# Optimization experiments

Hardware: AMD Instinct MI355X
Metric: run time of the kernel (lower is better)

Reference implementation:

```python
import jax, jax.numpy as jnp
import numpy as np

C = 256
CQK = C // 8  # query/key channels from Conv2d(in_dim, in_dim//8, 1)


def _cross_attn(x, y, qw, qb, kw, kb, vw, vb, gamma):
    # x, y: [B, C, H, W]; 1x1 convs are channel matmuls
    B, Cc, H, W = x.shape
    N = H * W
    xf = x.reshape(B, Cc, N)
    yf = y.reshape(B, Cc, N)
    q = jnp.einsum('oc,bcn->bno', qw, xf) + qb  # [B, N, CQK]
    k = jnp.einsum('oc,bcn->bon', kw, yf) + kb[:, None]  # [B, CQK, N]
    energy = jnp.einsum('bnc,bcm->bnm', q, k)  # [B, N, N]
    attn = jax.nn.softmax(energy, axis=2)
    v = jnp.einsum('oc,bcn->bon', vw, yf) + vb[:, None]  # [B, C, N]
    out = jnp.einsum('bcm,bnm->bcn', v, attn)  # value @ attention^T
    out = out.reshape(B, Cc, H, W)
    return gamma * out + x


def setup_inputs() -> dict:
    key = jax.random.key(0)
    ks = jax.random.split(key, 16)
    B, H, W = 4, 64, 64
    s = 1.0 / np.sqrt(C)
    d = {
        'x': jax.random.normal(ks[0], (B, C, H, W), jnp.float32),
        'y': jax.random.normal(ks[1], (B, C, H, W), jnp.float32),
        'z': jax.random.normal(ks[2], (B, C, H, W), jnp.float32),
        'q1_w': jax.random.normal(ks[3], (CQK, C), jnp.float32) * s,
        'q1_b': jax.random.normal(ks[4], (CQK,), jnp.float32) * s,
        'k1_w': jax.random.normal(ks[5], (CQK, C), jnp.float32) * s,
        'k1_b': jax.random.normal(ks[6], (CQK,), jnp.float32) * s,
        'v1_w': jax.random.normal(ks[7], (C, C), jnp.float32) * s,
        'v1_b': jax.random.normal(ks[8], (C,), jnp.float32) * s,
        'gamma1': jax.random.normal(ks[9], (1,), jnp.float32) * 0.1,
        'q2_w': jax.random.normal(ks[10], (CQK, C), jnp.float32) * s,
        'q2_b': jax.random.normal(ks[11], (CQK,), jnp.float32) * s,
        'k2_w': jax.random.normal(ks[12], (CQK, C), jnp.float32) * s,
        'k2_b': jax.random.normal(ks[13], (CQK,), jnp.float32) * s,
        'v2_w': jax.random.normal(ks[14], (C, C), jnp.float32) * s,
        'v2_b': jax.random.normal(ks[15], (C,), jnp.float32) * s,
        'gamma2': jax.random.normal(jax.random.fold_in(key, 99), (1,), jnp.float32) * 0.1,
    }
    return d


def reference(x, y, z, q1_w, q1_b, k1_w, k1_b, v1_w, v1_b, gamma1,
              q2_w, q2_b, k2_w, k2_b, v2_w, v2_b, gamma2):
    out1 = _cross_attn(x, y, q1_w, q1_b, k1_w, k1_b, v1_w, v1_b, gamma1)
    out2 = _cross_attn(out1, z, q2_w, q2_b, k2_w, k2_b, v2_w, v2_b, gamma2)
    return out2
```

## Files before the change

### kernel.cpp

```cpp
#include <hip/hip_runtime.h>
#include <hip/hip_bf16.h>

#define NSEQ 4096
#define CDIM 256
#define CQKD 32
#define LOG2E 1.4426950408889634f

typedef float v4f __attribute__((ext_vector_type(4)));
typedef float v16f __attribute__((ext_vector_type(16)));
typedef short v8s __attribute__((ext_vector_type(8)));
typedef unsigned long long u64;

__device__ __forceinline__ float exp2_(float x) {
#if __has_builtin(__builtin_amdgcn_exp2f)
  return __builtin_amdgcn_exp2f(x);
#else
  float r;
  __asm__("v_exp_f32 %0, %1" : "=v"(r) : "v"(x));
  return r;
#endif
}

__device__ __forceinline__ unsigned short f2bf(float x) {
  unsigned u = __builtin_bit_cast(unsigned, x);
  unsigned r = (u + 0x7FFFu + ((u >> 16) & 1u)) >> 16;
  return (unsigned short)r;
}
__device__ __forceinline__ float bf2f(unsigned short s) {
  unsigned u = ((unsigned)s) << 16;
  return __builtin_bit_cast(float, u);
}
__device__ __forceinline__ unsigned int pack_bf16(float a, float b) {
#if __has_builtin(__builtin_amdgcn_cvt_pk_bf16_f32)
  typedef __bf16 v2bf __attribute__((ext_vector_type(2)));
  v2bf r = __builtin_amdgcn_cvt_pk_bf16_f32(a, b);
  return __builtin_bit_cast(unsigned int, r);
#else
  return ((unsigned)f2bf(b) << 16) | (unsigned)f2bf(a);
#endif
}

__device__ __forceinline__ unsigned char f2e4m3(float x) {
  unsigned u = __builtin_bit_cast(unsigned, x);
  unsigned s = (u >> 24) & 0x80u;
  unsigned au = u & 0x7fffffffu;
  if (au > 0x43e00000u) return (unsigned char)(s | 0x7eu);
  if (au < 0x3c800000u) {
    float ax = __builtin_bit_cast(float, au);
    int q = (int)(ax * 512.0f + 0.5f);
    if (q > 7) q = 7;
    return (unsigned char)(s | (unsigned)q);
  }
  int e = (int)((au >> 23) & 0xffu) - 127 + 7;
  unsigned m = au & 0x7fffffu;
  unsigned mr = m + 0x7ffffu + ((m >> 20) & 1u);
  if (mr >= 0x800000u) { mr -= 0x800000u; e += 1; if (e >= 16) return (unsigned char)(s | 0x7e); }
  return (unsigned char)(s | ((unsigned)e << 3) | (mr >> 20));
}
__device__ __forceinline__ unsigned int pack4_fp8(float a, float b, float c, float d) {
#if __has_builtin(__builtin_amdgcn_cvt_pk_fp8_f32)
  int v = 0;
  v = __builtin_amdgcn_cvt_pk_fp8_f32(a, b, v, false);
  v = __builtin_amdgcn_cvt_pk_fp8_f32(c, d, v, true);
  return (unsigned int)v;
#else
  return (unsigned)f2e4m3(a) | ((unsigned)f2e4m3(b) << 8) |
         ((unsigned)f2e4m3(c) << 16) | ((unsigned)f2e4m3(d) << 24);
#endif
}

__device__ __forceinline__ void barrier_lds() {
  __asm__ __volatile__("s_waitcnt lgkmcnt(0)\n\ts_barrier" ::: "memory");
}

__global__ __launch_bounds__(256) void convw_kernel(
    const float* __restrict__ q1w, const float* __restrict__ k1w,
    const float* __restrict__ k2w, const float* __restrict__ q2w,
    const float* __restrict__ v1w, const float* __restrict__ v2w,
    unsigned short* __restrict__ W) {
  const int s = blockIdx.x * 256 + threadIdx.x;
  const float* src;
  int o, ch0;
  size_t obase;
  float scale = 1.0f;
  if (s < 3072) {
    const int wsel = s >> 10, r = s & 1023;
    src = wsel == 0 ? q1w : (wsel == 1 ? k1w : k2w);
    const int ot = r >> 9, cb = (r >> 6) & 7, lane = r & 63;
    o = ot * 16 + (lane & 15);
    ch0 = cb * 32 + ((lane >> 4) & 3) * 8;
    obase = (size_t)wsel * 8192 + (size_t)r * 8;
  } else if (s < 19456) {
    const int s2 = s - 3072, which = s2 >> 13, r = s2 & 8191;
    src = which == 0 ? v1w : v2w;
    const int ot = r >> 9, cb = (r >> 6) & 7, lane = r & 63;
    o = ot * 16 + (lane & 15);
    ch0 = cb * 32 + ((lane >> 4) & 3) * 8;
    obase = 32768 + (size_t)which * 65536 + (size_t)r * 8;
  } else {
    const int r = s - 19456;
    src = q2w;
    const int lane = r & 63;
    o = lane & 31;
    ch0 = (r >> 6) * 16 + (lane >> 5) * 8;
    obase = 24576 + (size_t)r * 8;
    scale = LOG2E;
  }
#pragma unroll
  for (int j = 0; j < 8; ++j)
    W[obase + j] = f2bf(src[o * CDIM + ch0 + j] * scale);
}

__global__ __launch_bounds__(256) void prep_kernel(
    const float* __restrict__ x, const float* __restrict__ y,
    const float* __restrict__ z, const unsigned short* __restrict__ Wbf,
    const float* __restrict__ q1b, const float* __restrict__ k1b,
    const float* __restrict__ k2b, const float* __restrict__ v1b,
    const float* __restrict__ v2b, unsigned short* __restrict__ Q1,
    unsigned short* __restrict__ K1, unsigned short* __restrict__ K2,
    unsigned char* __restrict__ V1, unsigned char* __restrict__ V2) {
  __shared__ unsigned short t[256][72];
  __shared__ unsigned short Kt[64][40];
  const int src = blockIdx.z;
  const float* in = src == 0 ? x : (src == 1 ? y : z);
  const int b = blockIdx.y;
  const int n0 = blockIdx.x * 64;
  const int tid = threadIdx.x, lane = tid & 63, w = tid >> 6;
  const int quad = lane >> 4, r15 = lane & 15, l31 = lane & 31, lh = lane >> 5;
  const float* ip = in + (size_t)(b * CDIM) * NSEQ + n0;
  {
    const int chb = tid >> 4, c4 = (tid & 15) * 4;
#pragma unroll
    for (int p = 0; p < 16; ++p) {
      const int ch = p * 16 + chb;
      float4 v = *(const float4*)(ip + (size_t)ch * NSEQ + c4);
      uint2 pk;
      pk.x = pack_bf16(v.x, v.y);
      pk.y = pack_bf16(v.z, v.w);
      *(uint2*)&t[ch][c4] = pk;
    }
  }
  __syncthreads();
  v8s af[8];
#pragma unroll
  for (int cb = 0; cb < 8; ++cb) {
    union { unsigned short e[8]; v8s v; } u;
#pragma unroll
    for (int j = 0; j < 8; ++j) u.e[j] = t[cb * 32 + quad * 8 + j][w * 16 + r15];
    af[cb] = u.v;
  }
  const int nt = blockIdx.x * 4 + w;
  const unsigned short* Wqk = Wbf + src * 8192;
  v4f a0 = {0.f, 0.f, 0.f, 0.f}, a1 = a0;
#pragma unroll
  for (int cb = 0; cb < 8; ++cb) {
    v8s b0 = *(const v8s*)(Wqk + (size_t)cb * 512 + lane * 8);
    v8s b1 = *(const v8s*)(Wqk + (size_t)(8 + cb) * 512 + lane * 8);
    a0 = __builtin_amdgcn_mfma_f32_16x16x32_bf16(af[cb], b0, a0, 0, 0, 0);
    a1 = __builtin_amdgcn_mfma_f32_16x16x32_bf16(af[cb], b1, a1, 0, 0, 0);
  }
  if (src == 0) {
#pragma unroll
    for (int r = 0; r < 4; ++r) {
      Q1[((size_t)b * NSEQ + nt * 16 + quad * 4 + r) * CQKD + r15] =
          f2bf((a0[r] + q1b[r15]) * LOG2E);
      Q1[((size_t)b * NSEQ + nt * 16 + quad * 4 + r) * CQKD + 16 + r15] =
          f2bf((a1[r] + q1b[16 + r15]) * LOG2E);
    }
    return;
  }
  const float* kbias = src == 1 ? k1b : k2b;
#pragma unroll
  for (int r = 0; r < 4; ++r) {
    Kt[w * 16 + quad * 4 + r][r15] = f2bf(a0[r] + kbias[r15]);
    Kt[w * 16 + quad * 4 + r][16 + r15] = f2bf(a1[r] + kbias[16 + r15]);
  }
  const unsigned short* Wv = Wbf + 32768 + (src - 1) * 65536;
  const float* vbias = src == 1 ? v1b : v2b;
  v4f vacc[16];
#pragma unroll
  for (int ot = 0; ot < 16; ++ot) vacc[ot] = (v4f){0.f, 0.f, 0.f, 0.f};
#pragma unroll
  for (int cb = 0; cb < 8; ++cb) {
    const v8s afc = af[cb];
#pragma unroll
    for (int ot = 0; ot < 16; ++ot) {
      v8s bf = *(const v8s*)(Wv + (size_t)(ot * 8 + cb) * 512 + lane * 8);
      vacc[ot] = __builtin_amdgcn_mfma_f32_16x16x32_bf16(afc, bf, vacc[ot], 0, 0, 0);
    }
  }
  __syncthreads();
  unsigned char* Vt8 = (unsigned char*)t;
#pragma unroll
  for (int ot = 0; ot < 16; ++ot) {
    const int ch = ot * 16 + r15;
    const float bv = vbias[ch];
    *(unsigned int*)&Vt8[(size_t)ch * 72 + w * 16 + quad * 4] =
        pack4_fp8(vacc[ot][0] + bv, vacc[ot][1] + bv, vacc[ot][2] + bv, vacc[ot][3] + bv);
  }
  {
    unsigned short* Kout = (src == 1 ? K1 : K2) + (size_t)b * (NSEQ / 16) * 512;
    *(v8s*)(Kout + ((size_t)nt * 64 + lane) * 8) = *(const v8s*)&Kt[w * 16 + r15][quad * 8];
  }
  __syncthreads();
  unsigned char* Vout = (src == 1 ? V1 : V2) + (size_t)b * (NSEQ / 16) * 8 * 512;
#pragma unroll
  for (int chb = 0; chb < 8; ++chb)
    *(u64*)(Vout + (((size_t)nt * 8 + chb) * 64 + lane) * 8) =
        *(const u64*)&Vt8[(size_t)(chb * 32 + l31) * 72 + w * 16 + lh * 8];
}


__device__ __forceinline__ void max_pass16(
    const unsigned short* __restrict__ Kp, const v8s qf[4], int w, int lane,
    float (*lbuf)[64], float m[4]) {
  const v4f vzero4 = {0.f, 0.f, 0.f, 0.f};
  const int r15 = lane & 15;
  const unsigned short* Kl = Kp + (size_t)w * 512 + lane * 8;
  v8s kA = *(const v8s*)(Kl);
  v8s kB = *(const v8s*)(Kl + 8192);
#pragma unroll
  for (int qt = 0; qt < 4; ++qt) m[qt] = -3.0e38f;
#pragma unroll 2
  for (int kt = 0; kt < 16; ++kt) {
    v8s kC = *(const v8s*)(Kl + (size_t)((kt + 2) & 15) * 8192);
#pragma unroll
    for (int qt = 0; qt < 4; ++qt) {
      v4f st = __builtin_amdgcn_mfma_f32_16x16x32_bf16(kA, qf[qt], vzero4, 0, 0, 0);
      m[qt] = fmaxf(m[qt], fmaxf(fmaxf(st[0], st[1]), fmaxf(st[2], st[3])));
    }
    kA = kB;
    kB = kC;
  }
#pragma unroll
  for (int qt = 0; qt < 4; ++qt) {
    m[qt] = fmaxf(m[qt], __shfl_xor(m[qt], 16));
    m[qt] = fmaxf(m[qt], __shfl_xor(m[qt], 32));
  }
  if (lane < 16) {
#pragma unroll
    for (int qt = 0; qt < 4; ++qt) lbuf[w][qt * 16 + lane] = m[qt];
  }
  __syncthreads();
#pragma unroll
  for (int qt = 0; qt < 4; ++qt) {
    float mm = lbuf[0][qt * 16 + r15];
#pragma unroll
    for (int ww = 1; ww < 16; ++ww) mm = fmaxf(mm, lbuf[ww][qt * 16 + r15]);
    m[qt] = mm;
  }
  __syncthreads();
}

__device__ __forceinline__ void s_phase(
    unsigned char* __restrict__ P, int pbuf, const v8s kf, const v8s qf[4],
    const float m[4], int w, int lane, float lsum[4]) {
  const v4f vzero4 = {0.f, 0.f, 0.f, 0.f};
  const int quad = lane >> 4, r15 = lane & 15;
  unsigned char* pw = P + pbuf * 8704 + w * 16 + quad * 4;
#pragma unroll
  for (int qt = 0; qt < 4; ++qt) {
    v4f st = __builtin_amdgcn_mfma_f32_16x16x32_bf16(kf, qf[qt], vzero4, 0, 0, 0);
    float e0 = exp2_(st[0] - m[qt]), e1 = exp2_(st[1] - m[qt]);
    float e2 = exp2_(st[2] - m[qt]), e3 = exp2_(st[3] - m[qt]);
    lsum[qt] += (e0 + e1) + (e2 + e3);
    *(unsigned int*)(pw + (size_t)(qt * 16 + r15) * 136) = pack4_fp8(e0, e1, e2, e3);
  }
}

__device__ __forceinline__ void attn_loop(
    const unsigned short* __restrict__ Kp, const unsigned char* __restrict__ Vp,
    unsigned char* __restrict__ P, const v8s qf[4], const float m[4], int w, int lane,
    v16f acc[2], float lsum[4]) {
  if (w < 8) {
    const unsigned short* Kl = Kp + (size_t)w * 512 + lane * 8;
    v8s kA = *(const v8s*)(Kl);
    v8s kB = *(const v8s*)(Kl + 4096);
    s_phase(P, 0, kA, qf, m, w, lane, lsum);
    barrier_lds();
#pragma unroll 2
    for (int t = 0; t < 32; ++t) {
      v8s kC = *(const v8s*)(Kl + (size_t)((t + 2) & 31) * 4096);
      if (t < 31) s_phase(P, (t + 1) & 1, kB, qf, m, w, lane, lsum);
      kA = kB;
      kB = kC;
      barrier_lds();
    }
  } else {
    const int l31 = lane & 31, lh = lane >> 5;
    const unsigned char* Vl = Vp + (size_t)(w - 8) * 512 + lane * 8;
    u64 vA[8], vB[8];
#pragma unroll
    for (int s = 0; s < 8; ++s) vA[s] = *(const u64*)(Vl + (size_t)s * 4096);
    barrier_lds();
#pragma unroll 2
    for (int t = 0; t < 32; ++t) {
#pragma unroll
      for (int s = 0; s < 8; ++s)
        vB[s] = *(const u64*)(Vl + (size_t)((t + 1) & 31) * 32768 + s * 4096);
      const unsigned char* pb = P + (t & 1) * 8704;
#pragma unroll
      for (int s = 0; s < 8; ++s) {
        long pf0 = (long)*(const u64*)(pb + (size_t)l31 * 136 + s * 16 + lh * 8);
        long pf1 = (long)*(const u64*)(pb + (size_t)(32 + l31) * 136 + s * 16 + lh * 8);
        acc[0] = __builtin_amdgcn_mfma_f32_32x32x16_fp8_fp8((long)vA[s], pf0, acc[0], 0, 0, 0);
        acc[1] = __builtin_amdgcn_mfma_f32_32x32x16_fp8_fp8((long)vA[s], pf1, acc[1], 0, 0, 0);
      }
#pragma unroll
      for (int s = 0; s < 8; ++s) vA[s] = vB[s];
      barrier_lds();
    }
  }
}

__global__ __launch_bounds__(1024, 4) void fused_attn_kernel(
    const unsigned short* __restrict__ Q1g, const unsigned short* __restrict__ K1g,
    const unsigned char* __restrict__ V1g, const unsigned short* __restrict__ K2g,
    const unsigned char* __restrict__ V2g, const unsigned short* __restrict__ W2g,
    const float* __restrict__ x, const float* __restrict__ q2b,
    const float* __restrict__ g1p, const float* __restrict__ g2p,
    float* __restrict__ outp) {
  __shared__ __align__(16) unsigned char P[2 * 8704];
  __shared__ __align__(16) unsigned short out1T[64 * 264];
  __shared__ __align__(16) unsigned short q2s[64 * 32];
  __shared__ float lbuf[16][64];

  const int tid = threadIdx.x;
  const int lane = tid & 63;
  const int w = tid >> 6;
  const int quad = lane >> 4;
  const int r15 = lane & 15;
  const int l31 = lane & 31, lh = lane >> 5;
  const int b = blockIdx.x & 3;
  const int n0 = (blockIdx.x >> 2) * 64;

  const float g1 = g1p[0];
  const float g2 = g2p[0];

  const unsigned short* Qp  = Q1g + (size_t)b * NSEQ * CQKD;
  const unsigned short* K1p = K1g + (size_t)b * (NSEQ / 16) * 512;
  const unsigned short* K2p = K2g + (size_t)b * (NSEQ / 16) * 512;
  const unsigned char* V1p  = V1g + (size_t)b * (NSEQ / 16) * 8 * 512;
  const unsigned char* V2p  = V2g + (size_t)b * (NSEQ / 16) * 8 * 512;

  v8s qf[4];
#pragma unroll
  for (int qt = 0; qt < 4; ++qt)
    qf[qt] = *(const v8s*)(Qp + (n0 + qt * 16 + r15) * CQKD + quad * 8);

  v16f acc[2];
  float lsum[4] = {0.f, 0.f, 0.f, 0.f};
  float m[4];
  acc[0] = (v16f)(0.f); acc[1] = (v16f)(0.f);

  max_pass16(K1p, qf, w, lane, lbuf, m);
  attn_loop(K1p, V1p, P, qf, m, w, lane, acc, lsum);
  if (w < 8) {
#pragma unroll
    for (int qt = 0; qt < 4; ++qt) {
      lsum[qt] += __shfl_xor(lsum[qt], 16);
      lsum[qt] += __shfl_xor(lsum[qt], 32);
    }
    if (lane < 16) {
#pragma unroll
      for (int qt = 0; qt < 4; ++qt) lbuf[w][qt * 16 + lane] = lsum[qt];
    }
  }
  __syncthreads();
  float rinv[2];
#pragma unroll
  for (int qh = 0; qh < 2; ++qh) {
    const int q = qh * 32 + l31;
    float d = 0.f;
#pragma unroll
    for (int ww = 0; ww < 8; ++ww) d += lbuf[ww][q];
    rinv[qh] = 1.0f / d;
  }
  if (w >= 8) {
    const int cw = (w - 8) * 32;
#pragma unroll
    for (int qh = 0; qh < 2; ++qh) {
      const int q = qh * 32 + l31;
#pragma unroll
      for (int rg = 0; rg < 4; ++rg) {
        const int c = cw + 8 * rg + 4 * lh;
        float o0 = g1 * (acc[qh][rg * 4 + 0] * rinv[qh]) + x[((size_t)b * CDIM + c + 0) * NSEQ + n0 + q];
        float o1 = g1 * (acc[qh][rg * 4 + 1] * rinv[qh]) + x[((size_t)b * CDIM + c + 1) * NSEQ + n0 + q];
        float o2 = g1 * (acc[qh][rg * 4 + 2] * rinv[qh]) + x[((size_t)b * CDIM + c + 2) * NSEQ + n0 + q];
        float o3 = g1 * (acc[qh][rg * 4 + 3] * rinv[qh]) + x[((size_t)b * CDIM + c + 3) * NSEQ + n0 + q];
        uint2 pk;
        pk.x = pack_bf16(o0, o1);
        pk.y = pack_bf16(o2, o3);
        *(uint2*)(out1T + (size_t)q * 264 + c) = pk;
      }
    }
  }
  __syncthreads();

  if (w < 2) {
    const int qh = w;
    v16f qacc = (v16f)(0.f);
#pragma unroll
    for (int s = 0; s < 16; ++s) {
      v8s af = *(const v8s*)(W2g + (size_t)(s * 64 + lane) * 8);
      v8s bf = *(const v8s*)(out1T + (size_t)(qh * 32 + l31) * 264 + s * 16 + lh * 8);
      qacc = __builtin_amdgcn_mfma_f32_32x32x16_bf16(af, bf, qacc, 0, 0, 0);
    }
#pragma unroll
    for (int rg = 0; rg < 4; ++rg) {
      const int o = 8 * rg + 4 * lh;
      uint2 pk;
      pk.x = pack_bf16(qacc[rg * 4 + 0] + q2b[o + 0] * LOG2E, qacc[rg * 4 + 1] + q2b[o + 1] * LOG2E);
      pk.y = pack_bf16(qacc[rg * 4 + 2] + q2b[o + 2] * LOG2E, qacc[rg * 4 + 3] + q2b[o + 3] * LOG2E);
      *(uint2*)(q2s + (size_t)(qh * 32 + l31) * 32 + o) = pk;
    }
  }
  __syncthreads();

#pragma unroll
  for (int qt = 0; qt < 4; ++qt)
    qf[qt] = *(const v8s*)(q2s + (qt * 16 + r15) * 32 + quad * 8);
  acc[0] = (v16f)(0.f); acc[1] = (v16f)(0.f);
#pragma unroll
  for (int qt = 0; qt < 4; ++qt) lsum[qt] = 0.f;
  max_pass16(K2p, qf, w, lane, lbuf, m);
  attn_loop(K2p, V2p, P, qf, m, w, lane, acc, lsum);
  if (w < 8) {
#pragma unroll
    for (int qt = 0; qt < 4; ++qt) {
      lsum[qt] += __shfl_xor(lsum[qt], 16);
      lsum[qt] += __shfl_xor(lsum[qt], 32);
    }
    if (lane < 16) {
#pragma unroll
      for (int qt = 0; qt < 4; ++qt) lbuf[w][qt * 16 + lane] = lsum[qt];
    }
  }
  __syncthreads();
#pragma unroll
  for (int qh = 0; qh < 2; ++qh) {
    const int q = qh * 32 + l31;
    float d = 0.f;
#pragma unroll
    for (int ww = 0; ww < 8; ++ww) d += lbuf[ww][q];
    rinv[qh] = 1.0f / d;
  }
  if (w >= 8) {
    const int cw = (w - 8) * 32;
#pragma unroll
    for (int qh = 0; qh < 2; ++qh) {
      const int q = qh * 32 + l31;
#pragma unroll
      for (int rg = 0; rg < 4; ++rg) {
        const int c = cw + 8 * rg + 4 * lh;
#pragma unroll
        for (int i = 0; i < 4; ++i) {
          float res = bf2f(out1T[(size_t)q * 264 + c + i]);
          outp[((size_t)b * CDIM + c + i) * NSEQ + n0 + q] =
              g2 * (acc[qh][rg * 4 + i] * rinv[qh]) + res;
        }
      }
    }
  }
}

extern "C" void kernel_launch(void* const* d_in, const int* in_sizes, int n_in,
                              void* d_out, int out_size, void* d_ws, size_t ws_size,
                              hipStream_t stream) {
  const float* x   = (const float*)d_in[0];
  const float* y   = (const float*)d_in[1];
  const float* z   = (const float*)d_in[2];
  const float* q1w = (const float*)d_in[3];
  const float* q1b = (const float*)d_in[4];
  const float* k1w = (const float*)d_in[5];
  const float* k1b = (const float*)d_in[6];
  const float* v1w = (const float*)d_in[7];
  const float* v1b = (const float*)d_in[8];
  const float* g1  = (const float*)d_in[9];
  const float* q2w = (const float*)d_in[10];
  const float* q2b = (const float*)d_in[11];
  const float* k2w = (const float*)d_in[12];
  const float* k2b = (const float*)d_in[13];
  const float* v2w = (const float*)d_in[14];
  const float* v2b = (const float*)d_in[15];
  const float* g2  = (const float*)d_in[16];
  char* ws = (char*)d_ws;
  unsigned short* Wbf = (unsigned short*)(ws);
  unsigned short* Q1  = (unsigned short*)(ws + 327680);
  unsigned short* K1  = (unsigned short*)(ws + 1376256);
  unsigned short* K2  = (unsigned short*)(ws + 2424832);
  unsigned char*  V1  = (unsigned char*)(ws + 3473408);
  unsigned char*  V2  = (unsigned char*)(ws + 7667712);
  float* outp = (float*)d_out;

  convw_kernel<<<dim3(80), 256, 0, stream>>>(q1w, k1w, k2w, q2w, v1w, v2w, Wbf);
  prep_kernel<<<dim3(64, 4, 3), 256, 0, stream>>>(x, y, z, Wbf, q1b, k1b, k2b, v1b,
                                                  v2b, Q1, K1, K2, V1, V2);
  fused_attn_kernel<<<dim3(256), 1024, 0, stream>>>(Q1, K1, V1, K2, V2, Wbf + 24576, x,
                                                    q2b, g1, g2, outp);
}
```

Measured before the change: 214.2 us.

## Merge weight conversion, projection prep and attention into one cooperative kernel

Replaces the three launches (weight conversion, Q/K/V projection, fused attention) with one cooperative kernel of 256 blocks × 1024 threads that uses grid.sync between phases. The projection phase runs three 256-thread groups per block, one each for x, y and z, on the same 64-token tile, and splits the V accumulation into two halves to limit register pressure. This aims to remove launch gaps and tail effects between kernels. In exchange it adds grid-wide barriers, drops the min-blocks hint from launch bounds, and uses about 123 KB of static shared memory for every phase, which may limit occupancy or co-residency.

```diff
diff --git a/kernel.cpp b/kernel.cpp
--- a/kernel.cpp
+++ b/kernel.cpp
@@ -1,5 +1,6 @@
 #include <hip/hip_runtime.h>
 #include <hip/hip_bf16.h>
+#include <hip/hip_cooperative_groups.h>
 
 #define NSEQ 4096
 #define CDIM 256
@@ -72,144 +73,6 @@
 __device__ __forceinline__ void barrier_lds() {
   __asm__ __volatile__("s_waitcnt lgkmcnt(0)\n\ts_barrier" ::: "memory");
 }
-
-__global__ __launch_bounds__(256) void convw_kernel(
-    const float* __restrict__ q1w, const float* __restrict__ k1w,
-    const float* __restrict__ k2w, const float* __restrict__ q2w,
-    const float* __restrict__ v1w, const float* __restrict__ v2w,
-    unsigned short* __restrict__ W) {
-  const int s = blockIdx.x * 256 + threadIdx.x;
-  const float* src;
-  int o, ch0;
-  size_t obase;
-  float scale = 1.0f;
-  if (s < 3072) {
-    const int wsel = s >> 10, r = s & 1023;
-    src = wsel == 0 ? q1w : (wsel == 1 ? k1w : k2w);
-    const int ot = r >> 9, cb = (r >> 6) & 7, lane = r & 63;
-    o = ot * 16 + (lane & 15);
-    ch0 = cb * 32 + ((lane >> 4) & 3) * 8;
-    obase = (size_t)wsel * 8192 + (size_t)r * 8;
-  } else if (s < 19456) {
-    const int s2 = s - 3072, which = s2 >> 13, r = s2 & 8191;
-    src = which == 0 ? v1w : v2w;
-    const int ot = r >> 9, cb = (r >> 6) & 7, lane = r & 63;
-    o = ot * 16 + (lane & 15);
-    ch0 = cb * 32 + ((lane >> 4) & 3) * 8;
-    obase = 32768 + (size_t)which * 65536 + (size_t)r * 8;
-  } else {
-    const int r = s - 19456;
-    src = q2w;
-    const int lane = r & 63;
-    o = lane & 31;
-    ch0 = (r >> 6) * 16 + (lane >> 5) * 8;
-    obase = 24576 + (size_t)r * 8;
-    scale = LOG2E;
-  }
-#pragma unroll
-  for (int j = 0; j < 8; ++j)
-    W[obase + j] = f2bf(src[o * CDIM + ch0 + j] * scale);
-}
-
-__global__ __launch_bounds__(256) void prep_kernel(
-    const float* __restrict__ x, const float* __restrict__ y,
-    const float* __restrict__ z, const unsigned short* __restrict__ Wbf,
-    const float* __restrict__ q1b, const float* __restrict__ k1b,
-    const float* __restrict__ k2b, const float* __restrict__ v1b,
-    const float* __restrict__ v2b, unsigned short* __restrict__ Q1,
-    unsigned short* __restrict__ K1, unsigned short* __restrict__ K2,
-    unsigned char* __restrict__ V1, unsigned char* __restrict__ V2) {
-  __shared__ unsigned short t[256][72];
-  __shared__ unsigned short Kt[64][40];
-  const int src = blockIdx.z;
-  const float* in = src == 0 ? x : (src == 1 ? y : z);
-  const int b = blockIdx.y;
-  const int n0 = blockIdx.x * 64;
-  const int tid = threadIdx.x, lane = tid & 63, w = tid >> 6;
-  const int quad = lane >> 4, r15 = lane & 15, l31 = lane & 31, lh = lane >> 5;
-  const float* ip = in + (size_t)(b * CDIM) * NSEQ + n0;
-  {
-    const int chb = tid >> 4, c4 = (tid & 15) * 4;
-#pragma unroll
-    for (int p = 0; p < 16; ++p) {
-      const int ch = p * 16 + chb;
-      float4 v = *(const float4*)(ip + (size_t)ch * NSEQ + c4);
-      uint2 pk;
-      pk.x = pack_bf16(v.x, v.y);
-      pk.y = pack_bf16(v.z, v.w);
-      *(uint2*)&t[ch][c4] = pk;
-    }
-  }
-  __syncthreads();
-  v8s af[8];
-#pragma unroll
-  for (int cb = 0; cb < 8; ++cb) {
-    union { unsigned short e[8]; v8s v; } u;
-#pragma unroll
-    for (int j = 0; j < 8; ++j) u.e[j] = t[cb * 32 + quad * 8 + j][w * 16 + r15];
-    af[cb] = u.v;
-  }
-  const int nt = blockIdx.x * 4 + w;
-  const unsigned short* Wqk = Wbf + src * 8192;
-  v4f a0 = {0.f, 0.f, 0.f, 0.f}, a1 = a0;
-#pragma unroll
-  for (int cb = 0; cb < 8; ++cb) {
-    v8s b0 = *(const v8s*)(Wqk + (size_t)cb * 512 + lane * 8);
-    v8s b1 = *(const v8s*)(Wqk + (size_t)(8 + cb) * 512 + lane * 8);
-    a0 = __builtin_amdgcn_mfma_f32_16x16x32_bf16(af[cb], b0, a0, 0, 0, 0);
-    a1 = __builtin_amdgcn_mfma_f32_16x16x32_bf16(af[cb], b1, a1, 0, 0, 0);
-  }
-  if (src == 0) {
-#pragma unroll
-    for (int r = 0; r < 4; ++r) {
-      Q1[((size_t)b * NSEQ + nt * 16 + quad * 4 + r) * CQKD + r15] =
-          f2bf((a0[r] + q1b[r15]) * LOG2E);
-      Q1[((size_t)b * NSEQ + nt * 16 + quad * 4 + r) * CQKD + 16 + r15] =
-          f2bf((a1[r] + q1b[16 + r15]) * LOG2E);
-    }
-    return;
-  }
-  const float* kbias = src == 1 ? k1b : k2b;
-#pragma unroll
-  for (int r = 0; r < 4; ++r) {
-    Kt[w * 16 + quad * 4 + r][r15] = f2bf(a0[r] + kbias[r15]);
-    Kt[w * 16 + quad * 4 + r][16 + r15] = f2bf(a1[r] + kbias[16 + r15]);
-  }
-  const unsigned short* Wv = Wbf + 32768 + (src - 1) * 65536;
-  const float* vbias = src == 1 ? v1b : v2b;
-  v4f vacc[16];
-#pragma unroll
-  for (int ot = 0; ot < 16; ++ot) vacc[ot] = (v4f){0.f, 0.f, 0.f, 0.f};
-#pragma unroll
-  for (int cb = 0; cb < 8; ++cb) {
-    const v8s afc = af[cb];
-#pragma unroll
-    for (int ot = 0; ot < 16; ++ot) {
-      v8s bf = *(const v8s*)(Wv + (size_t)(ot * 8 + cb) * 512 + lane * 8);
-      vacc[ot] = __builtin_amdgcn_mfma_f32_16x16x32_bf16(afc, bf, vacc[ot], 0, 0, 0);
-    }
-  }
-  __syncthreads();
-  unsigned char* Vt8 = (unsigned char*)t;
-#pragma unroll
-  for (int ot = 0; ot < 16; ++ot) {
-    const int ch = ot * 16 + r15;
-    const float bv = vbias[ch];
-    *(unsigned int*)&Vt8[(size_t)ch * 72 + w * 16 + quad * 4] =
-        pack4_fp8(vacc[ot][0] + bv, vacc[ot][1] + bv, vacc[ot][2] + bv, vacc[ot][3] + bv);
-  }
-  {
-    unsigned short* Kout = (src == 1 ? K1 : K2) + (size_t)b * (NSEQ / 16) * 512;
-    *(v8s*)(Kout + ((size_t)nt * 64 + lane) * 8) = *(const v8s*)&Kt[w * 16 + r15][quad * 8];
-  }
-  __syncthreads();
-  unsigned char* Vout = (src == 1 ? V1 : V2) + (size_t)b * (NSEQ / 16) * 8 * 512;
-#pragma unroll
-  for (int chb = 0; chb < 8; ++chb)
-    *(u64*)(Vout + (((size_t)nt * 8 + chb) * 64 + lane) * 8) =
-        *(const u64*)&Vt8[(size_t)(chb * 32 + l31) * 72 + w * 16 + lh * 8];
-}
-
 
 __device__ __forceinline__ void max_pass16(
     const unsigned short* __restrict__ Kp, const v8s qf[4], int w, int lane,
@@ -313,151 +176,304 @@
   }
 }
 
-__global__ __launch_bounds__(1024, 4) void fused_attn_kernel(
-    const unsigned short* __restrict__ Q1g, const unsigned short* __restrict__ K1g,
-    const unsigned char* __restrict__ V1g, const unsigned short* __restrict__ K2g,
-    const unsigned char* __restrict__ V2g, const unsigned short* __restrict__ W2g,
-    const float* __restrict__ x, const float* __restrict__ q2b,
-    const float* __restrict__ g1p, const float* __restrict__ g2p,
+__global__ __launch_bounds__(1024) void mega_kernel(
+    const float* __restrict__ x, const float* __restrict__ y, const float* __restrict__ z,
+    const float* __restrict__ q1w, const float* __restrict__ q1b,
+    const float* __restrict__ k1w, const float* __restrict__ k1b,
+    const float* __restrict__ v1w, const float* __restrict__ v1b,
+    const float* __restrict__ g1p,
+    const float* __restrict__ q2w, const float* __restrict__ q2b,
+    const float* __restrict__ k2w, const float* __restrict__ k2b,
+    const float* __restrict__ v2w, const float* __restrict__ v2b,
+    const float* __restrict__ g2p,
+    unsigned short* __restrict__ Wbf, unsigned short* __restrict__ Q1,
+    unsigned short* __restrict__ K1, unsigned short* __restrict__ K2,
+    unsigned char* __restrict__ V1, unsigned char* __restrict__ V2,
     float* __restrict__ outp) {
-  __shared__ __align__(16) unsigned char P[2 * 8704];
-  __shared__ __align__(16) unsigned short out1T[64 * 264];
-  __shared__ __align__(16) unsigned short q2s[64 * 32];
-  __shared__ float lbuf[16][64];
-
+  __shared__ __align__(16) char smem[125952];
   const int tid = threadIdx.x;
-  const int lane = tid & 63;
-  const int w = tid >> 6;
-  const int quad = lane >> 4;
-  const int r15 = lane & 15;
-  const int l31 = lane & 31, lh = lane >> 5;
   const int b = blockIdx.x & 3;
   const int n0 = (blockIdx.x >> 2) * 64;
-
-  const float g1 = g1p[0];
-  const float g2 = g2p[0];
-
-  const unsigned short* Qp  = Q1g + (size_t)b * NSEQ * CQKD;
-  const unsigned short* K1p = K1g + (size_t)b * (NSEQ / 16) * 512;
-  const unsigned short* K2p = K2g + (size_t)b * (NSEQ / 16) * 512;
-  const unsigned char* V1p  = V1g + (size_t)b * (NSEQ / 16) * 8 * 512;
-  const unsigned char* V2p  = V2g + (size_t)b * (NSEQ / 16) * 8 * 512;
-
-  v8s qf[4];
-#pragma unroll
-  for (int qt = 0; qt < 4; ++qt)
-    qf[qt] = *(const v8s*)(Qp + (n0 + qt * 16 + r15) * CQKD + quad * 8);
-
-  v16f acc[2];
-  float lsum[4] = {0.f, 0.f, 0.f, 0.f};
-  float m[4];
-  acc[0] = (v16f)(0.f); acc[1] = (v16f)(0.f);
-
-  max_pass16(K1p, qf, w, lane, lbuf, m);
-  attn_loop(K1p, V1p, P, qf, m, w, lane, acc, lsum);
-  if (w < 8) {
-#pragma unroll
-    for (int qt = 0; qt < 4; ++qt) {
-      lsum[qt] += __shfl_xor(lsum[qt], 16);
-      lsum[qt] += __shfl_xor(lsum[qt], 32);
-    }
-    if (lane < 16) {
-#pragma unroll
-      for (int qt = 0; qt < 4; ++qt) lbuf[w][qt * 16 + lane] = lsum[qt];
-    }
-  }
-  __syncthreads();
-  float rinv[2];
-#pragma unroll
-  for (int qh = 0; qh < 2; ++qh) {
-    const int q = qh * 32 + l31;
-    float d = 0.f;
-#pragma unroll
-    for (int ww = 0; ww < 8; ++ww) d += lbuf[ww][q];
-    rinv[qh] = 1.0f / d;
-  }
-  if (w >= 8) {
-    const int cw = (w - 8) * 32;
+  cooperative_groups::grid_group grid = cooperative_groups::this_grid();
+
+  {
+    const int s = blockIdx.x * 1024 + tid;
+    if (s < 20480) {
+      const float* src;
+      int o, ch0;
+      size_t obase;
+      float scale = 1.0f;
+      if (s < 3072) {
+        const int wsel = s >> 10, r = s & 1023;
+        src = wsel == 0 ? q1w : (wsel == 1 ? k1w : k2w);
+        const int ot = r >> 9, cb = (r >> 6) & 7, lane = r & 63;
+        o = ot * 16 + (lane & 15);
+        ch0 = cb * 32 + ((lane >> 4) & 3) * 8;
+        obase = (size_t)wsel * 8192 + (size_t)r * 8;
+      } else if (s < 19456) {
+        const int s2 = s - 3072, which = s2 >> 13, r = s2 & 8191;
+        src = which == 0 ? v1w : v2w;
+        const int ot = r >> 9, cb = (r >> 6) & 7, lane = r & 63;
+        o = ot * 16 + (lane & 15);
+        ch0 = cb * 32 + ((lane >> 4) & 3) * 8;
+        obase = 32768 + (size_t)which * 65536 + (size_t)r * 8;
+      } else {
+        const int r = s - 19456;
+        src = q2w;
+        const int lane = r & 63;
+        o = lane & 31;
+        ch0 = (r >> 6) * 16 + (lane >> 5) * 8;
+        obase = 24576 + (size_t)r * 8;
+        scale = LOG2E;
+      }
+#pragma unroll
+      for (int j = 0; j < 8; ++j)
+        Wbf[obase + j] = f2bf(src[o * CDIM + ch0 + j] * scale);
+    }
+  }
+  __threadfence();
+  grid.sync();
+
+  {
+    const int src = tid >> 8;
+    const int ptid = tid & 255;
+    const int lane = ptid & 63, wp = ptid >> 6;
+    const int quad = lane >> 4, r15 = lane & 15, l31 = lane & 31, lh = lane >> 5;
+    unsigned short (*t)[72] = (unsigned short (*)[72])(smem + (src < 3 ? src : 0) * 41984);
+    unsigned short (*Kt)[40] = (unsigned short (*)[40])(smem + (src < 3 ? src : 0) * 41984 + 36864);
+    if (src < 3) {
+      const float* in = src == 0 ? x : (src == 1 ? y : z);
+      const float* ip = in + (size_t)(b * CDIM) * NSEQ + n0;
+      const int chb = ptid >> 4, c4 = (ptid & 15) * 4;
+#pragma unroll
+      for (int p = 0; p < 16; ++p) {
+        const int ch = p * 16 + chb;
+        float4 v = *(const float4*)(ip + (size_t)ch * NSEQ + c4);
+        uint2 pk;
+        pk.x = pack_bf16(v.x, v.y);
+        pk.y = pack_bf16(v.z, v.w);
+        *(uint2*)&t[ch][c4] = pk;
+      }
+    }
+    __syncthreads();
+    v8s af[8];
+    if (src < 3) {
+#pragma unroll
+      for (int cb = 0; cb < 8; ++cb) {
+        union { unsigned short e[8]; v8s v; } u;
+#pragma unroll
+        for (int j = 0; j < 8; ++j) u.e[j] = t[cb * 32 + quad * 8 + j][wp * 16 + r15];
+        af[cb] = u.v;
+      }
+    }
+    __syncthreads();
+    if (src < 3) {
+      const int nt = (blockIdx.x >> 2) * 4 + wp;
+      const unsigned short* Wqk = Wbf + src * 8192;
+      v4f a0 = {0.f, 0.f, 0.f, 0.f}, a1 = a0;
+#pragma unroll
+      for (int cb = 0; cb < 8; ++cb) {
+        v8s b0 = *(const v8s*)(Wqk + (size_t)cb * 512 + lane * 8);
+        v8s b1 = *(const v8s*)(Wqk + (size_t)(8 + cb) * 512 + lane * 8);
+        a0 = __builtin_amdgcn_mfma_f32_16x16x32_bf16(af[cb], b0, a0, 0, 0, 0);
+        a1 = __builtin_amdgcn_mfma_f32_16x16x32_bf16(af[cb], b1, a1, 0, 0, 0);
+      }
+      if (src == 0) {
+#pragma unroll
+        for (int r = 0; r < 4; ++r) {
+          Q1[((size_t)b * NSEQ + nt * 16 + quad * 4 + r) * CQKD + r15] =
+              f2bf((a0[r] + q1b[r15]) * LOG2E);
+          Q1[((size_t)b * NSEQ + nt * 16 + quad * 4 + r) * CQKD + 16 + r15] =
+              f2bf((a1[r] + q1b[16 + r15]) * LOG2E);
+        }
+      } else {
+        const float* kbias = src == 1 ? k1b : k2b;
+#pragma unroll
+        for (int r = 0; r < 4; ++r) {
+          Kt[wp * 16 + quad * 4 + r][r15] = f2bf(a0[r] + kbias[r15]);
+          Kt[wp * 16 + quad * 4 + r][16 + r15] = f2bf(a1[r] + kbias[16 + r15]);
+        }
+        const unsigned short* Wv = Wbf + 32768 + (src - 1) * 65536;
+        const float* vbias = src == 1 ? v1b : v2b;
+        unsigned char* Vt8 = (unsigned char*)t;
+#pragma unroll 1
+        for (int half = 0; half < 2; ++half) {
+          v4f vacc[8];
+#pragma unroll
+          for (int o2 = 0; o2 < 8; ++o2) vacc[o2] = (v4f){0.f, 0.f, 0.f, 0.f};
+#pragma unroll
+          for (int cb = 0; cb < 8; ++cb) {
+            const v8s afc = af[cb];
+#pragma unroll
+            for (int o2 = 0; o2 < 8; ++o2) {
+              v8s bfr = *(const v8s*)(Wv + (size_t)((half * 8 + o2) * 8 + cb) * 512 + lane * 8);
+              vacc[o2] = __builtin_amdgcn_mfma_f32_16x16x32_bf16(afc, bfr, vacc[o2], 0, 0, 0);
+            }
+          }
+#pragma unroll
+          for (int o2 = 0; o2 < 8; ++o2) {
+            const int ch = (half * 8 + o2) * 16 + r15;
+            const float bv = vbias[ch];
+            *(unsigned int*)&Vt8[(size_t)ch * 72 + wp * 16 + quad * 4] =
+                pack4_fp8(vacc[o2][0] + bv, vacc[o2][1] + bv, vacc[o2][2] + bv, vacc[o2][3] + bv);
+          }
+        }
+        unsigned short* Kout = (src == 1 ? K1 : K2) + (size_t)b * (NSEQ / 16) * 512;
+        *(v8s*)(Kout + ((size_t)nt * 64 + lane) * 8) = *(const v8s*)&Kt[wp * 16 + r15][quad * 8];
+      }
+    }
+    __syncthreads();
+    if (src == 1 || src == 2) {
+      const int nt = (blockIdx.x >> 2) * 4 + wp;
+      unsigned char* Vt8 = (unsigned char*)t;
+      unsigned char* Vout = (src == 1 ? V1 : V2) + (size_t)b * (NSEQ / 16) * 8 * 512;
+#pragma unroll
+      for (int chb = 0; chb < 8; ++chb)
+        *(u64*)(Vout + (((size_t)nt * 8 + chb) * 64 + lane) * 8) =
+            *(const u64*)&Vt8[(size_t)(chb * 32 + l31) * 72 + wp * 16 + lh * 8];
+    }
+  }
+  __threadfence();
+  grid.sync();
+
+  {
+    unsigned char* P = (unsigned char*)smem;
+    unsigned short* out1T = (unsigned short*)(smem + 17408);
+    unsigned short* q2s = (unsigned short*)(smem + 51200);
+    float (*lbuf)[64] = (float (*)[64])(smem + 55296);
+
+    const int lane = tid & 63;
+    const int w = tid >> 6;
+    const int quad = lane >> 4;
+    const int r15 = lane & 15;
+    const int l31 = lane & 31, lh = lane >> 5;
+
+    const float g1 = g1p[0];
+    const float g2 = g2p[0];
+
+    const unsigned short* Qp  = Q1 + (size_t)b * NSEQ * CQKD;
+    const unsigned short* K1p = K1 + (size_t)b * (NSEQ / 16) * 512;
+    const unsigned short* K2p = K2 + (size_t)b * (NSEQ / 16) * 512;
+    const unsigned char* V1p  = V1 + (size_t)b * (NSEQ / 16) * 8 * 512;
+    const unsigned char* V2p  = V2 + (size_t)b * (NSEQ / 16) * 8 * 512;
+    const unsigned short* W2g = Wbf + 24576;
+
+    v8s qf[4];
+#pragma unroll
+    for (int qt = 0; qt < 4; ++qt)
+      qf[qt] = *(const v8s*)(Qp + (n0 + qt * 16 + r15) * CQKD + quad * 8);
+
+    v16f acc[2];
+    float lsum[4] = {0.f, 0.f, 0.f, 0.f};
+    float m[4];
+    acc[0] = (v16f)(0.f); acc[1] = (v16f)(0.f);
+
+    max_pass16(K1p, qf, w, lane, lbuf, m);
+    attn_loop(K1p, V1p, P, qf, m, w, lane, acc, lsum);
+    if (w < 8) {
+#pragma unroll
+      for (int qt = 0; qt < 4; ++qt) {
+        lsum[qt] += __shfl_xor(lsum[qt], 16);
+        lsum[qt] += __shfl_xor(lsum[qt], 32);
+      }
+      if (lane < 16) {
+#pragma unroll
+        for (int qt = 0; qt < 4; ++qt) lbuf[w][qt * 16 + lane] = lsum[qt];
+      }
+    }
+    __syncthreads();
+    float rinv[2];
 #pragma unroll
     for (int qh = 0; qh < 2; ++qh) {
       const int q = qh * 32 + l31;
+      float d = 0.f;
+#pragma unroll
+      for (int ww = 0; ww < 8; ++ww) d += lbuf[ww][q];
+      rinv[qh] = 1.0f / d;
+    }
+    if (w >= 8) {
+      const int cw = (w - 8) * 32;
+#pragma unroll
+      for (int qh = 0; qh < 2; ++qh) {
+        const int q = qh * 32 + l31;
+#pragma unroll
+        for (int rg = 0; rg < 4; ++rg) {
+          const int c = cw + 8 * rg + 4 * lh;
+          float o0 = g1 * (acc[qh][rg * 4 + 0] * rinv[qh]) + x[((size_t)b * CDIM + c + 0) * NSEQ + n0 + q];
+          float o1 = g1 * (acc[qh][rg * 4 + 1] * rinv[qh]) + x[((size_t)b * CDIM + c + 1) * NSEQ + n0 + q];
+          float o2 = g1 * (acc[qh][rg * 4 + 2] * rinv[qh]) + x[((size_t)b * CDIM + c + 2) * NSEQ + n0 + q];
+          float o3 = g1 * (acc[qh][rg * 4 + 3] * rinv[qh]) + x[((size_t)b * CDIM + c + 3) * NSEQ + n0 + q];
+          uint2 pk;
+          pk.x = pack_bf16(o0, o1);
+          pk.y = pack_bf16(o2, o3);
+          *(uint2*)(out1T + (size_t)q * 264 + c) = pk;
+        }
+      }
+    }
+    __syncthreads();
+
+    if (w < 2) {
+      const int qh = w;
+      v16f qacc = (v16f)(0.f);
+#pragma unroll
+      for (int s = 0; s < 16; ++s) {
+        v8s af = *(const v8s*)(W2g + (size_t)(s * 64 + lane) * 8);
+        v8s bfr = *(const v8s*)(out1T + (size_t)(qh * 32 + l31) * 264 + s * 16 + lh * 8);
+        qacc = __builtin_amdgcn_mfma_f32_32x32x16_bf16(af, bfr, qacc, 0, 0, 0);
+      }
 #pragma unroll
       for (int rg = 0; rg < 4; ++rg) {
-        const int c = cw + 8 * rg + 4 * lh;
-        float o0 = g1 * (acc[qh][rg * 4 + 0] * rinv[qh]) + x[((size_t)b * CDIM + c + 0) * NSEQ + n0 + q];
-        float o1 = g1 * (acc[qh][rg * 4 + 1] * rinv[qh]) + x[((size_t)b * CDIM + c + 1) * NSEQ + n0 + q];
-        float o2 = g1 * (acc[qh][rg * 4 + 2] * rinv[qh]) + x[((size_t)b * CDIM + c + 2) * NSEQ + n0 + q];
-        float o3 = g1 * (acc[qh][rg * 4 + 3] * rinv[qh]) + x[((size_t)b * CDIM + c + 3) * NSEQ + n0 + q];
+        const int o = 8 * rg + 4 * lh;
         uint2 pk;
-        pk.x = pack_bf16(o0, o1);
-        pk.y = pack_bf16(o2, o3);
-        *(uint2*)(out1T + (size_t)q * 264 + c) = pk;
-      }
-    }
-  }
-  __syncthreads();
-
-  if (w < 2) {
-    const int qh = w;
-    v16f qacc = (v16f)(0.f);
-#pragma unroll
-    for (int s = 0; s < 16; ++s) {
-      v8s af = *(const v8s*)(W2g + (size_t)(s * 64 + lane) * 8);
-      v8s bf = *(const v8s*)(out1T + (size_t)(qh * 32 + l31) * 264 + s * 16 + lh * 8);
-      qacc = __builtin_amdgcn_mfma_f32_32x32x16_bf16(af, bf, qacc, 0, 0, 0);
-    }
-#pragma unroll
-    for (int rg = 0; rg < 4; ++rg) {
-      const int o = 8 * rg + 4 * lh;
-      uint2 pk;
-      pk.x = pack_bf16(qacc[rg * 4 + 0] + q2b[o + 0] * LOG2E, qacc[rg * 4 + 1] + q2b[o + 1] * LOG2E);
-      pk.y = pack_bf16(qacc[rg * 4 + 2] + q2b[o + 2] * LOG2E, qacc[rg * 4 + 3] + q2b[o + 3] * LOG2E);
-      *(uint2*)(q2s + (size_t)(qh * 32 + l31) * 32 + o) = pk;
-    }
-  }
-  __syncthreads();
-
-#pragma unroll
-  for (int qt = 0; qt < 4; ++qt)
-    qf[qt] = *(const v8s*)(q2s + (qt * 16 + r15) * 32 + quad * 8);
-  acc[0] = (v16f)(0.f); acc[1] = (v16f)(0.f);
-#pragma unroll
-  for (int qt = 0; qt < 4; ++qt) lsum[qt] = 0.f;
-  max_pass16(K2p, qf, w, lane, lbuf, m);
-  attn_loop(K2p, V2p, P, qf, m, w, lane, acc, lsum);
-  if (w < 8) {
-#pragma unroll
-    for (int qt = 0; qt < 4; ++qt) {
-      lsum[qt] += __shfl_xor(lsum[qt], 16);
-      lsum[qt] += __shfl_xor(lsum[qt], 32);
-    }
-    if (lane < 16) {
-#pragma unroll
-      for (int qt = 0; qt < 4; ++qt) lbuf[w][qt * 16 + lane] = lsum[qt];
-    }
-  }
-  __syncthreads();
-#pragma unroll
-  for (int qh = 0; qh < 2; ++qh) {
-    const int q = qh * 32 + l31;
-    float d = 0.f;
-#pragma unroll
-    for (int ww = 0; ww < 8; ++ww) d += lbuf[ww][q];
-    rinv[qh] = 1.0f / d;
-  }
-  if (w >= 8) {
-    const int cw = (w - 8) * 32;
+        pk.x = pack_bf16(qacc[rg * 4 + 0] + q2b[o + 0] * LOG2E, qacc[rg * 4 + 1] + q2b[o + 1] * LOG2E);
+        pk.y = pack_bf16(qacc[rg * 4 + 2] + q2b[o + 2] * LOG2E, qacc[rg * 4 + 3] + q2b[o + 3] * LOG2E);
+        *(uint2*)(q2s + (size_t)(qh * 32 + l31) * 32 + o) = pk;
+      }
+    }
+    __syncthreads();
+
+#pragma unroll
+    for (int qt = 0; qt < 4; ++qt)
+      qf[qt] = *(const v8s*)(q2s + (qt * 16 + r15) * 32 + quad * 8);
+    acc[0] = (v16f)(0.f); acc[1] = (v16f)(0.f);
+#pragma unroll
+    for (int qt = 0; qt < 4; ++qt) lsum[qt] = 0.f;
+    max_pass16(K2p, qf, w, lane, lbuf, m);
+    attn_loop(K2p, V2p, P, qf, m, w, lane, acc, lsum);
+    if (w < 8) {
+#pragma unroll
+      for (int qt = 0; qt < 4; ++qt) {
+        lsum[qt] += __shfl_xor(lsum[qt], 16);
+        lsum[qt] += __shfl_xor(lsum[qt], 32);
+      }
+      if (lane < 16) {
+#pragma unroll
+        for (int qt = 0; qt < 4; ++qt) lbuf[w][qt * 16 + lane] = lsum[qt];
+      }
+    }
+    __syncthreads();
 #pragma unroll
     for (int qh = 0; qh < 2; ++qh) {
       const int q = qh * 32 + l31;
-#pragma unroll
-      for (int rg = 0; rg < 4; ++rg) {
-        const int c = cw + 8 * rg + 4 * lh;
-#pragma unroll
-        for (int i = 0; i < 4; ++i) {
-          float res = bf2f(out1T[(size_t)q * 264 + c + i]);
-          outp[((size_t)b * CDIM + c + i) * NSEQ + n0 + q] =
-              g2 * (acc[qh][rg * 4 + i] * rinv[qh]) + res;
+      float d = 0.f;
+#pragma unroll
+      for (int ww = 0; ww < 8; ++ww) d += lbuf[ww][q];
+      rinv[qh] = 1.0f / d;
+    }
+    if (w >= 8) {
+      const int cw = (w - 8) * 32;
+#pragma unroll
+      for (int qh = 0; qh < 2; ++qh) {
+        const int q = qh * 32 + l31;
+#pragma unroll
+        for (int rg = 0; rg < 4; ++rg) {
+          const int c = cw + 8 * rg + 4 * lh;
+#pragma unroll
+          for (int i = 0; i < 4; ++i) {
+            float res = bf2f(out1T[(size_t)q * 264 + c + i]);
+            outp[((size_t)b * CDIM + c + i) * NSEQ + n0 + q] =
+                g2 * (acc[qh][rg * 4 + i] * rinv[qh]) + res;
+          }
         }
       }
     }
@@ -493,9 +509,11 @@
   unsigned char*  V2  = (unsigned char*)(ws + 7667712);
   float* outp = (float*)d_out;
 
-  convw_kernel<<<dim3(80), 256, 0, stream>>>(q1w, k1w, k2w, q2w, v1w, v2w, Wbf);
-  prep_kernel<<<dim3(64, 4, 3), 256, 0, stream>>>(x, y, z, Wbf, q1b, k1b, k2b, v1b,
-                                                  v2b, Q1, K1, K2, V1, V2);
-  fused_attn_kernel<<<dim3(256), 1024, 0, stream>>>(Q1, K1, V1, K2, V2, Wbf + 24576, x,
-                                                    q2b, g1, g2, outp);
-}
+  void* args[] = {(void*)&x,   (void*)&y,   (void*)&z,   (void*)&q1w, (void*)&q1b,
+                  (void*)&k1w, (void*)&k1b, (void*)&v1w, (void*)&v1b, (void*)&g1,
+                  (void*)&q2w, (void*)&q2b, (void*)&k2w, (void*)&k2b, (void*)&v2w,
+                  (void*)&v2b, (void*)&g2,  (void*)&Wbf, (void*)&Q1,  (void*)&K1,
+                  (void*)&K2,  (void*)&V1,  (void*)&V2,  (void*)&outp};
+  hipLaunchCooperativeKernel((const void*)mega_kernel, dim3(256), dim3(1024), args, 0,
+                             stream);
+}
```

Result: slower. 470.8 us (+119.8%).

## Process two key tiles per barrier with four P buffers and MFMA priority

Applied to the files above, without the earlier changes.

The producer/consumer attention loop now handles two 64-key tiles per barrier instead of one, using four P staging buffers in LDS instead of two. This halves the number of block-wide barriers in the S/PV pipeline. The PV warps raise their scheduling priority around the MFMA sequence via s_setprio. LDS use grows by about 17KB, which may reduce occupancy, and the doubled V register prefetch buffers add register pressure.

```diff
diff --git a/kernel.cpp b/kernel.cpp
--- a/kernel.cpp
+++ b/kernel.cpp
@@ -268,48 +268,69 @@
   }
 }
 
+__device__ __forceinline__ void pv_tile(
+    const unsigned char* __restrict__ P, int pbuf, const u64 vf[8], int lane,
+    v16f acc[2]) {
+  const int l31 = lane & 31, lh = lane >> 5;
+  const unsigned char* pb = P + pbuf * 8704;
+  __builtin_amdgcn_s_setprio(1);
+#pragma unroll
+  for (int s = 0; s < 8; ++s) {
+    long pf0 = (long)*(const u64*)(pb + (size_t)l31 * 136 + s * 16 + lh * 8);
+    long pf1 = (long)*(const u64*)(pb + (size_t)(32 + l31) * 136 + s * 16 + lh * 8);
+    acc[0] = __builtin_amdgcn_mfma_f32_32x32x16_fp8_fp8((long)vf[s], pf0, acc[0], 0, 0, 0);
+    acc[1] = __builtin_amdgcn_mfma_f32_32x32x16_fp8_fp8((long)vf[s], pf1, acc[1], 0, 0, 0);
+  }
+  __builtin_amdgcn_s_setprio(0);
+}
+
 __device__ __forceinline__ void attn_loop(
     const unsigned short* __restrict__ Kp, const unsigned char* __restrict__ Vp,
     unsigned char* __restrict__ P, const v8s qf[4], const float m[4], int w, int lane,
     v16f acc[2], float lsum[4]) {
   if (w < 8) {
     const unsigned short* Kl = Kp + (size_t)w * 512 + lane * 8;
-    v8s kA = *(const v8s*)(Kl);
-    v8s kB = *(const v8s*)(Kl + 4096);
-    s_phase(P, 0, kA, qf, m, w, lane, lsum);
+    v8s k0 = *(const v8s*)(Kl);
+    v8s k1 = *(const v8s*)(Kl + 4096);
+    s_phase(P, 0, k0, qf, m, w, lane, lsum);
+    k0 = *(const v8s*)(Kl + 2 * 4096);
+    s_phase(P, 1, k1, qf, m, w, lane, lsum);
+    k1 = *(const v8s*)(Kl + 3 * 4096);
     barrier_lds();
-#pragma unroll 2
-    for (int t = 0; t < 32; ++t) {
-      v8s kC = *(const v8s*)(Kl + (size_t)((t + 2) & 31) * 4096);
-      if (t < 31) s_phase(P, (t + 1) & 1, kB, qf, m, w, lane, lsum);
-      kA = kB;
-      kB = kC;
+#pragma unroll 1
+    for (int p = 1; p < 16; ++p) {
+      const int bs = (p & 1) * 2;
+      s_phase(P, bs, k0, qf, m, w, lane, lsum);
+      k0 = *(const v8s*)(Kl + (size_t)((2 * p + 2) & 31) * 4096);
+      s_phase(P, bs + 1, k1, qf, m, w, lane, lsum);
+      k1 = *(const v8s*)(Kl + (size_t)((2 * p + 3) & 31) * 4096);
       barrier_lds();
     }
+    barrier_lds();
   } else {
-    const int l31 = lane & 31, lh = lane >> 5;
     const unsigned char* Vl = Vp + (size_t)(w - 8) * 512 + lane * 8;
-    u64 vA[8], vB[8];
-#pragma unroll
-    for (int s = 0; s < 8; ++s) vA[s] = *(const u64*)(Vl + (size_t)s * 4096);
+    u64 v0[8], v1[8];
+#pragma unroll
+    for (int s = 0; s < 8; ++s) v0[s] = *(const u64*)(Vl + (size_t)s * 4096);
+#pragma unroll
+    for (int s = 0; s < 8; ++s) v1[s] = *(const u64*)(Vl + 32768 + (size_t)s * 4096);
     barrier_lds();
-#pragma unroll 2
-    for (int t = 0; t < 32; ++t) {
+#pragma unroll 1
+    for (int p = 0; p < 15; ++p) {
+      const int bs = (p & 1) * 2;
+      pv_tile(P, bs, v0, lane, acc);
 #pragma unroll
       for (int s = 0; s < 8; ++s)
-        vB[s] = *(const u64*)(Vl + (size_t)((t + 1) & 31) * 32768 + s * 4096);
-      const unsigned char* pb = P + (t & 1) * 8704;
-#pragma unroll
-      for (int s = 0; s < 8; ++s) {
-        long pf0 = (long)*(const u64*)(pb + (size_t)l31 * 136 + s * 16 + lh * 8);
-        long pf1 = (long)*(const u64*)(pb + (size_t)(32 + l31) * 136 + s * 16 + lh * 8);
-        acc[0] = __builtin_amdgcn_mfma_f32_32x32x16_fp8_fp8((long)vA[s], pf0, acc[0], 0, 0, 0);
-        acc[1] = __builtin_amdgcn_mfma_f32_32x32x16_fp8_fp8((long)vA[s], pf1, acc[1], 0, 0, 0);
-      }
-#pragma unroll
-      for (int s = 0; s < 8; ++s) vA[s] = vB[s];
+        v0[s] = *(const u64*)(Vl + (size_t)(2 * p + 2) * 32768 + s * 4096);
+      pv_tile(P, bs + 1, v1, lane, acc);
+#pragma unroll
+      for (int s = 0; s < 8; ++s)
+        v1[s] = *(const u64*)(Vl + (size_t)(2 * p + 3) * 32768 + s * 4096);
       barrier_lds();
     }
+    pv_tile(P, 2, v0, lane, acc);
+    pv_tile(P, 3, v1, lane, acc);
+    barrier_lds();
   }
 }
 
@@ -320,7 +341,7 @@
     const float* __restrict__ x, const float* __restrict__ q2b,
     const float* __restrict__ g1p, const float* __restrict__ g2p,
     float* __restrict__ outp) {
-  __shared__ __align__(16) unsigned char P[2 * 8704];
+  __shared__ __align__(16) unsigned char P[4 * 8704];
   __shared__ __align__(16) unsigned short out1T[64 * 264];
   __shared__ __align__(16) unsigned short q2s[64 * 32];
   __shared__ float lbuf[16][64];
```

New measurement: 210.3 us (median of 2 runs). Within noise of the previous version (-1.8%).
